# Kernel optimization log

Measured on AMD Instinct MI355X. Metric: run time of the kernel, lower is better.

Reference implementation:

```python
import jax, jax.numpy as jnp
import numpy as np

H = 128             # hidden_channels (heads=1 in PyG HGTConv default)
NT, NC, NM = 150000, 40000, 10000   # transactions, customers, merchants
NE = 150000         # edges per base relation
L = 2               # num HGTConv layers
OUT = 2             # out_channels
# node types: 0=transaction, 1=customer, 2=merchant
EDGE_TYPES = ((1, 0), (2, 0), (0, 1), (0, 2))  # (src_type, dst_type)


def setup_inputs():
    key = jax.random.key(0)
    ks = jax.random.split(key, 20)
    s = 1.0 / np.sqrt(H)
    return {
        'x_tx': jax.random.normal(ks[0], (NT, 16), jnp.float32),
        'x_cust': jax.random.normal(ks[1], (NC, 32), jnp.float32),
        'merch_ids': jnp.arange(NM, dtype=jnp.int32),
        'e_ct_src': jax.random.randint(ks[2], (NE,), 0, NC, dtype=jnp.int32),
        'e_ct_dst': jax.random.randint(ks[3], (NE,), 0, NT, dtype=jnp.int32),
        'e_mt_src': jax.random.randint(ks[4], (NE,), 0, NM, dtype=jnp.int32),
        'e_mt_dst': jax.random.randint(ks[5], (NE,), 0, NT, dtype=jnp.int32),
        'proj_tx_w': jax.random.normal(ks[6], (16, H), jnp.float32) * 0.25,
        'proj_tx_b': jnp.zeros((H,), jnp.float32),
        'proj_cust_w': jax.random.normal(ks[7], (32, H), jnp.float32) * 0.18,
        'proj_cust_b': jnp.zeros((H,), jnp.float32),
        'merch_emb': jax.random.normal(ks[8], (NM, H), jnp.float32),
        'kw': jax.random.normal(ks[9], (L, 3, H, H), jnp.float32) * s,
        'kb': jnp.zeros((L, 3, H), jnp.float32),
        'qw': jax.random.normal(ks[10], (L, 3, H, H), jnp.float32) * s,
        'qb': jnp.zeros((L, 3, H), jnp.float32),
        'vw': jax.random.normal(ks[11], (L, 3, H, H), jnp.float32) * s,
        'vb': jnp.zeros((L, 3, H), jnp.float32),
        'aw': jax.random.normal(ks[12], (L, 3, H, H), jnp.float32) * s,
        'ab': jnp.zeros((L, 3, H), jnp.float32),
        'skip': jnp.ones((L, 3), jnp.float32),
        'a_rel': jax.random.normal(ks[13], (L, 4, H, H), jnp.float32) * s,
        'm_rel': jax.random.normal(ks[14], (L, 4, H, H), jnp.float32) * s,
        'p_rel': jnp.ones((L, 4), jnp.float32),
        'out_w': jax.random.normal(ks[15], (H, OUT), jnp.float32) * s,
        'out_b': jnp.zeros((OUT,), jnp.float32),
    }


def _segment_softmax(alpha, dst, n):
    m = jax.ops.segment_max(alpha, dst, num_segments=n)
    m = jnp.where(jnp.isfinite(m), m, 0.0)
    e = jnp.exp(alpha - m[dst])
    z = jax.ops.segment_sum(e, dst, num_segments=n)
    return e / (z[dst] + 1e-16)


def _hgt_conv(xs, lp, edges, sizes):
    kw, kb, qw, qb, vw, vb, aw, ab, skip, a_rel, m_rel, p_rel = lp
    k = [xs[t] @ kw[t] + kb[t] for t in range(3)]
    q = [xs[t] @ qw[t] + qb[t] for t in range(3)]
    v = [xs[t] @ vw[t] + vb[t] for t in range(3)]
    agg = [jnp.zeros_like(xs[t]) for t in range(3)]
    inv_sqrt_d = 1.0 / jnp.sqrt(jnp.float32(H))
    for r, (st, dt) in enumerate(EDGE_TYPES):
        src, dst = edges[r]
        k_e = (k[st] @ a_rel[r])[src]   # [E,H] relation-transformed keys at edge sources
        v_e = (v[st] @ m_rel[r])[src]   # [E,H]
        a = jnp.sum(q[dt][dst] * k_e, axis=-1) * p_rel[r] * inv_sqrt_d  # [E]
        a = _segment_softmax(a, dst, sizes[dt])
        agg[dt] = agg[dt] + jax.ops.segment_sum(a[:, None] * v_e, dst, num_segments=sizes[dt])
    out = []
    for t in range(3):
        o = jax.nn.gelu(agg[t], approximate=False) @ aw[t] + ab[t]
        beta = jax.nn.sigmoid(skip[t])
        out.append(beta * o + (1.0 - beta) * xs[t])
    return out


def _forward(x_tx, x_cust, proj_tx_w, proj_tx_b, proj_cust_w, proj_cust_b, merch_emb,
             kw, kb, qw, qb, vw, vb, aw, ab, skip, a_rel, m_rel, p_rel, out_w, out_b,
             merch_ids, edges):
    xs = [x_tx @ proj_tx_w + proj_tx_b,
          x_cust @ proj_cust_w + proj_cust_b,
          merch_emb[merch_ids]]
    sizes = (NT, NC, NM)
    for l in range(L):
        lp = (kw[l], kb[l], qw[l], qb[l], vw[l], vb[l], aw[l], ab[l], skip[l],
              a_rel[l], m_rel[l], p_rel[l])
        xs = _hgt_conv(xs, lp, edges, sizes)
        xs = [jax.nn.relu(x) for x in xs]   # dropout is identity in eval mode
    return xs[0] @ out_w + out_b            # logits on 'transaction' nodes


def reference(x_tx, x_cust, merch_ids, e_ct_src, e_ct_dst, e_mt_src, e_mt_dst,
              proj_tx_w, proj_tx_b, proj_cust_w, proj_cust_b, merch_emb,
              kw, kb, qw, qb, vw, vb, aw, ab, skip, a_rel, m_rel, p_rel, out_w, out_b):
    edges = ((e_ct_src, e_ct_dst), (e_mt_src, e_mt_dst),
             (e_ct_dst, e_ct_src), (e_mt_dst, e_mt_src))
    return _forward(x_tx, x_cust, proj_tx_w, proj_tx_b, proj_cust_w, proj_cust_b,
                    merch_emb, kw, kb, qw, qb, vw, vb, aw, ab, skip,
                    a_rel, m_rel, p_rel, out_w, out_b, merch_ids, edges)
```

## Files before the change

kernel.cpp:

```cpp
#include <hip/hip_runtime.h>
#include <math.h>

#define H 128
#define NTX 150000
#define NCU 40000
#define NME 10000
#define NEDGE 150000
#define NLAY 2
#define WC_STRIDE 33280
#define WKC_STRIDE 16640
#define BUF_FLOATS 19200000
#define AGG2_OFF 5120000
#define SCAN_TILE 2048

typedef short s8v __attribute__((ext_vector_type(8)));
typedef float f32x4 __attribute__((ext_vector_type(4)));

__device__ __forceinline__ float gelu_exact(float x) {
    return 0.5f * x * (1.0f + erff(x * 0.70710678118654752f));
}
__device__ __forceinline__ unsigned short f2bf(float x) {
    unsigned u = __float_as_uint(x);
    return (unsigned short)((u + 0x7FFFu + ((u >> 16) & 1u)) >> 16);
}
__device__ __forceinline__ float bf2f(unsigned short b) {
    return __uint_as_float(((unsigned)b) << 16);
}

__global__ __launch_bounds__(256) void fill_val(float* p, int n, float v) {
    int i = blockIdx.x * 256 + threadIdx.x;
    if (i < n) p[i] = v;
}
__global__ __launch_bounds__(256) void zero_int(int* p, int n) {
    int i = blockIdx.x * 256 + threadIdx.x;
    if (i < n) p[i] = 0;
}
__global__ __launch_bounds__(256) void copy_int(int* d, const int* s, int n) {
    int i = blockIdx.x * 256 + threadIdx.x;
    if (i < n) d[i] = s[i];
}

__global__ __launch_bounds__(256) void count_deg(const int* __restrict__ dst,
    int* __restrict__ deg, int E)
{
    int e = blockIdx.x * 256 + threadIdx.x;
    if (e < E) atomicAdd(&deg[dst[e]], 1);
}
__global__ __launch_bounds__(256) void scan1(const int* __restrict__ deg,
    int* __restrict__ out, int* __restrict__ bsum, int n)
{
    __shared__ int ts[256];
    int tid = threadIdx.x;
    int base = blockIdx.x * SCAN_TILE + tid * 8;
    int v[8], pre[8], s = 0;
    #pragma unroll
    for (int j = 0; j < 8; ++j) {
        int idx = base + j;
        v[j] = (idx < n) ? deg[idx] : 0;
        pre[j] = s; s += v[j];
    }
    ts[tid] = s;
    __syncthreads();
    for (int off = 1; off < 256; off <<= 1) {
        int t = (tid >= off) ? ts[tid - off] : 0;
        __syncthreads();
        ts[tid] += t;
        __syncthreads();
    }
    int excl = ts[tid] - s;
    #pragma unroll
    for (int j = 0; j < 8; ++j)
        if (base + j < n) out[base + j] = excl + pre[j];
    if (tid == 255) bsum[blockIdx.x] = ts[255];
}
__global__ __launch_bounds__(64) void scan2(int* __restrict__ bsum, int nb) {
    if (threadIdx.x == 0 && blockIdx.x == 0) {
        int run = 0;
        for (int i = 0; i < nb; ++i) { int t = bsum[i]; bsum[i] = run; run += t; }
    }
}
__global__ __launch_bounds__(256) void scan3(int* __restrict__ out,
    const int* __restrict__ bsum, int n, int total)
{
    int base = blockIdx.x * SCAN_TILE;
    int add = bsum[blockIdx.x];
    for (int j = threadIdx.x; j < SCAN_TILE; j += 256) {
        int k = base + j;
        if (k < n) out[k] += add;
    }
    if (blockIdx.x == 0 && threadIdx.x == 0) out[n] = total;
}
__global__ __launch_bounds__(256) void fill_csr(const int* __restrict__ src,
    const int* __restrict__ dst, int* __restrict__ cursor, int* __restrict__ col, int E)
{
    int e = blockIdx.x * 256 + threadIdx.x;
    if (e >= E) return;
    int pos = atomicAdd(&cursor[dst[e]], 1);
    col[pos] = src[e];
}

template<int K>
__global__ __launch_bounds__(256) void proj_kernel(const float* __restrict__ X,
    const float* __restrict__ W, const float* __restrict__ B,
    float* __restrict__ Y, int N)
{
    __shared__ float Wl[K][128];
    __shared__ float Bl[128];
    int tid = threadIdx.x;
    for (int i = tid; i < K * 128; i += 256) Wl[i >> 7][i & 127] = W[i];
    if (tid < 128) Bl[tid] = B[tid];
    __syncthreads();
    int ng = tid >> 5, lane = tid & 31;
    int n = blockIdx.x * 8 + ng;
    if (n >= N) return;
    const float* xr = X + (size_t)n * K;
    float xa[K];
    #pragma unroll
    for (int k4 = 0; k4 < K / 4; ++k4)
        *(float4*)&xa[k4 * 4] = *(const float4*)(xr + k4 * 4);
    int c0 = lane * 4;
    float4 acc = *(const float4*)&Bl[c0];
    #pragma unroll
    for (int k = 0; k < K; ++k) {
        float4 w = *(const float4*)&Wl[k][c0];
        acc.x += xa[k] * w.x; acc.y += xa[k] * w.y;
        acc.z += xa[k] * w.z; acc.w += xa[k] * w.w;
    }
    *(float4*)(Y + (size_t)n * H + c0) = acc;
}

__global__ __launch_bounds__(256) void gather_rows(const float* __restrict__ src,
    const int* __restrict__ ids, float* __restrict__ dstp, int N)
{
    int t = blockIdx.x * 256 + threadIdx.x;
    if (t >= N * 32) return;
    int n = t >> 5, c4 = t & 31;
    int sid = ids[n];
    ((float4*)dstp)[(size_t)n * 32 + c4] = ((const float4*)src)[(size_t)sid * 32 + c4];
}

__global__ __launch_bounds__(256) void combine1_par(const float* __restrict__ kw,
    const float* __restrict__ kb, const float* __restrict__ vw, const float* __restrict__ vb,
    const float* __restrict__ a_rel, const float* __restrict__ m_rel,
    float* __restrict__ wkc, float* __restrict__ wc)
{
    __shared__ float Rs[64][132];
    int b = blockIdx.x;
    int combo = b >> 3;
    int pass  = (b >> 2) & 1;
    int slice = b & 3;
    int l = combo >> 2, r = combo & 3;
    const int src_t[4] = {1, 2, 0, 0};
    int st = src_t[r];
    const float* Ap = (pass ? vw : kw) + (size_t)(l*3 + st) * H * H;
    const float* Rp = (pass ? m_rel : a_rel) + (size_t)combo * H * H;
    float* Out = pass ? (wc + (size_t)combo * WC_STRIDE + 16384)
                      : (wkc + (size_t)combo * WKC_STRIDE);

    int tid = threadIdx.x;
    int i = slice * 32 + (tid >> 3);
    int jb = tid & 7;
    float acc[16];
    #pragma unroll
    for (int j = 0; j < 16; ++j) acc[j] = 0.f;

    for (int half = 0; half < 2; ++half) {
        __syncthreads();
        for (int idx = tid; idx < 64 * 128; idx += 256)
            Rs[idx >> 7][idx & 127] = Rp[(half * 64 + (idx >> 7)) * H + (idx & 127)];
        __syncthreads();
        for (int k = 0; k < 64; ++k) {
            float a = Ap[i * H + half * 64 + k];
            #pragma unroll
            for (int j = 0; j < 16; ++j) acc[j] += a * Rs[k][jb + j * 8];
        }
    }
    #pragma unroll
    for (int j = 0; j < 16; ++j) Out[i * H + jb + j * 8] = acc[j];

    if (pass == 0 && slice == 0 && tid < 128) {
        const float* Avb = vb + (size_t)(l*3 + st) * H;
        const float* Rv = m_rel + (size_t)combo * H * H;
        float* bvc = wc + (size_t)combo * WC_STRIDE + 32896;
        float s = 0.f;
        for (int k = 0; k < H; ++k) s += Avb[k] * Rv[k * H + tid];
        bvc[tid] = s;
    }
}

__global__ __launch_bounds__(256) void combine2_par(const float* __restrict__ qw,
    const float* __restrict__ qb, const float* __restrict__ wkc, float* __restrict__ wc)
{
    __shared__ float BsT[64][133];
    int b = blockIdx.x;
    int combo = b >> 2;
    int slice = b & 3;
    int l = combo >> 2, r = combo & 3;
    const int dst_t[4] = {0, 0, 1, 2};
    int dt = dst_t[r];
    const float* Q  = qw + (size_t)(l*3 + dt) * H * H;
    const float* Qb = qb + (size_t)(l*3 + dt) * H;
    const float* WKc = wkc + (size_t)combo * WKC_STRIDE;
    float* QWc = wc + (size_t)combo * WC_STRIDE;

    int tid = threadIdx.x;
    int i = slice * 32 + (tid >> 3);
    int jb = tid & 7;
    float acc[16];
    #pragma unroll
    for (int j = 0; j < 16; ++j) acc[j] = 0.f;

    for (int half = 0; half < 2; ++half) {
        __syncthreads();
        for (int idx = tid; idx < 64 * 128; idx += 256) {
            int j = idx >> 6, k = idx & 63;
            BsT[k][j] = WKc[j * H + half * 64 + k];
        }
        __syncthreads();
        for (int k = 0; k < 64; ++k) {
            float a = Q[i * H + half * 64 + k];
            #pragma unroll
            for (int j = 0; j < 16; ++j) acc[j] += a * BsT[k][jb + j * 8];
        }
    }
    #pragma unroll
    for (int j = 0; j < 16; ++j) QWc[i * H + jb + j * 8] = acc[j];

    if (slice == 0 && tid < 128) {
        float* qbc = wc + (size_t)combo * WC_STRIDE + 32768;
        float s = 0.f;
        for (int k = 0; k < H; ++k) s += Qb[k] * WKc[tid * H + k];
        qbc[tid] = s;
    }
}

__global__ __launch_bounds__(256) void wprep(const float* __restrict__ wc,
    const float* __restrict__ aw, unsigned short* __restrict__ wt)
{
    int b = blockIdx.x;
    const float* src = (b < 16)
        ? wc + (size_t)(b >> 1) * WC_STRIDE + ((b & 1) ? 16384 : 0)
        : aw + (size_t)(b - 16) * 16384;
    unsigned short* hi = wt + (size_t)b * 32768;
    unsigned short* lo = hi + 16384;
    for (int idx = threadIdx.x; idx < 16384; idx += 256) {
        int k = idx >> 7, j = idx & 127;
        float w = src[idx];
        unsigned short h = f2bf(w);
        hi[j * 128 + k] = h;
        lo[j * 128 + k] = f2bf(w - bf2f(h));
    }
}

#define STAGE_TILE(SRC, GELU)                                               \
    _Pragma("unroll")                                                       \
    for (int i = 0; i < 8; ++i) {                                           \
        int u = tid + i * 256;                                              \
        int n = u >> 5, c4 = u & 31;                                        \
        int gn = nb + n;                                                    \
        float4 v = make_float4(0.f, 0.f, 0.f, 0.f);                         \
        if (gn < N) v = *(const float4*)((SRC) + (size_t)gn * H + c4 * 4);  \
        if (GELU) {                                                         \
            v.x = gelu_exact(v.x); v.y = gelu_exact(v.y);                   \
            v.z = gelu_exact(v.z); v.w = gelu_exact(v.w);                   \
        }                                                                   \
        ushort4 h, lo;                                                      \
        h.x = f2bf(v.x); lo.x = f2bf(v.x - bf2f(h.x));                      \
        h.y = f2bf(v.y); lo.y = f2bf(v.y - bf2f(h.y));                      \
        h.z = f2bf(v.z); lo.z = f2bf(v.z - bf2f(h.z));                      \
        h.w = f2bf(v.w); lo.w = f2bf(v.w - bf2f(h.w));                      \
        *(ushort4*)&lds[0][n][c4 * 4] = h;                                  \
        *(ushort4*)&lds[1][n][c4 * 4] = lo;                                 \
    }

#define LOAD_BFRAG(WT)                                                      \
    _Pragma("unroll")                                                       \
    for (int n = 0; n < 2; ++n) {                                           \
        int j = col0 + n * 16 + l15;                                        \
        _Pragma("unroll")                                                   \
        for (int kb = 0; kb < 4; ++kb) {                                    \
            bhi[n][kb] = *(const s8v*)((WT) + (size_t)j * 128 + kb * 32 + kg * 8);          \
            blo[n][kb] = *(const s8v*)((WT) + 16384 + (size_t)j * 128 + kb * 32 + kg * 8);  \
        }                                                                   \
    }

#define MFMA_PASS()                                                         \
    _Pragma("unroll")                                                       \
    for (int m = 0; m < 4; ++m) {                                           \
        int row = m * 16 + l15;                                             \
        _Pragma("unroll")                                                   \
        for (int kb = 0; kb < 4; ++kb) {                                    \
            s8v ah = *(const s8v*)&lds[0][row][kb * 32 + kg * 8];           \
            s8v al = *(const s8v*)&lds[1][row][kb * 32 + kg * 8];           \
            _Pragma("unroll")                                               \
            for (int n = 0; n < 2; ++n) {                                   \
                acc[m][n] = __builtin_amdgcn_mfma_f32_16x16x32_bf16(ah, bhi[n][kb], acc[m][n], 0, 0, 0); \
                acc[m][n] = __builtin_amdgcn_mfma_f32_16x16x32_bf16(al, bhi[n][kb], acc[m][n], 0, 0, 0); \
                acc[m][n] = __builtin_amdgcn_mfma_f32_16x16x32_bf16(ah, blo[n][kb], acc[m][n], 0, 0, 0); \
            }                                                               \
        }                                                                   \
    }

template<int MODE>
__global__ __launch_bounds__(256) void mfma_gemm(const float* __restrict__ X,
    const unsigned short* __restrict__ Wt, const float* __restrict__ Bias,
    float* __restrict__ Y, int N, const float* __restrict__ Xold,
    const float* __restrict__ skipP, const float* __restrict__ zb)
{
    __shared__ unsigned short lds[2][64][136];
    int tid = threadIdx.x;
    int nb = blockIdx.x * 64;

    STAGE_TILE(X, MODE == 1)
    __syncthreads();

    int wid = tid >> 6, lane = tid & 63;
    int l15 = lane & 15, kg = lane >> 4;
    int col0 = wid * 32;

    s8v bhi[2][4], blo[2][4];
    LOAD_BFRAG(Wt)

    f32x4 acc[4][2];
    #pragma unroll
    for (int m = 0; m < 4; ++m)
        #pragma unroll
        for (int n = 0; n < 2; ++n)
            acc[m][n] = (f32x4){0.f, 0.f, 0.f, 0.f};

    MFMA_PASS()

    float beta = 0.f, omb = 0.f;
    if (MODE == 1) {
        float s = *skipP;
        beta = 1.f / (1.f + expf(-s));
        omb = 1.f - beta;
    }
    float bias0 = Bias[col0 + l15];
    float bias1 = Bias[col0 + 16 + l15];

    #pragma unroll
    for (int m = 0; m < 4; ++m) {
        #pragma unroll
        for (int r = 0; r < 4; ++r) {
            int grow = nb + m * 16 + kg * 4 + r;
            if (grow < N) {
                float gate = 1.f;
                if (MODE == 3) gate = (zb[grow] > 0.f) ? 1.f : 0.f;
                #pragma unroll
                for (int n = 0; n < 2; ++n) {
                    int col = col0 + n * 16 + l15;
                    float val = acc[m][n][r];
                    float bs = n ? bias1 : bias0;
                    size_t yi = (size_t)grow * H + col;
                    if (MODE == 0) {
                        Y[yi] = val + bs;
                    } else if (MODE == 3) {
                        Y[yi] = val + gate * bs;
                    } else {
                        float o = val + bs;
                        float xo = Xold[yi];
                        Y[yi] = fmaxf(beta * o + omb * xo, 0.f);
                    }
                }
            }
        }
    }
}

__global__ __launch_bounds__(256) void mfma_gemm2q(const float* __restrict__ X,
    const unsigned short* __restrict__ Wt0, const unsigned short* __restrict__ Wt1,
    const float* __restrict__ b0, const float* __restrict__ b1,
    float* __restrict__ Y0, float* __restrict__ Y1, int N)
{
    __shared__ unsigned short lds[2][64][136];
    int tid = threadIdx.x;
    int nb = blockIdx.x * 64;

    STAGE_TILE(X, 0)
    __syncthreads();

    int wid = tid >> 6, lane = tid & 63;
    int l15 = lane & 15, kg = lane >> 4;
    int col0 = wid * 32;

    #pragma unroll
    for (int set = 0; set < 2; ++set) {
        const unsigned short* Wt = set ? Wt1 : Wt0;
        const float* Bias = set ? b1 : b0;
        float* Y = set ? Y1 : Y0;

        s8v bhi[2][4], blo[2][4];
        LOAD_BFRAG(Wt)

        f32x4 acc[4][2];
        #pragma unroll
        for (int m = 0; m < 4; ++m)
            #pragma unroll
            for (int n = 0; n < 2; ++n)
                acc[m][n] = (f32x4){0.f, 0.f, 0.f, 0.f};

        MFMA_PASS()

        float bias0 = Bias[col0 + l15];
        float bias1 = Bias[col0 + 16 + l15];
        #pragma unroll
        for (int m = 0; m < 4; ++m) {
            #pragma unroll
            for (int r = 0; r < 4; ++r) {
                int grow = nb + m * 16 + kg * 4 + r;
                if (grow < N) {
                    #pragma unroll
                    for (int n = 0; n < 2; ++n) {
                        int col = col0 + n * 16 + l15;
                        Y[(size_t)grow * H + col] = acc[m][n][r] + (n ? bias1 : bias0);
                    }
                }
            }
        }
    }
}

__global__ __launch_bounds__(256) void mfma_gemmV2(float* __restrict__ A0,
    const float* __restrict__ A1,
    const unsigned short* __restrict__ Wt0, const unsigned short* __restrict__ Wt1,
    const float* __restrict__ bv0, const float* __restrict__ bv1,
    const float* __restrict__ z0, const float* __restrict__ z1, int N)
{
    __shared__ unsigned short lds[2][64][136];
    int tid = threadIdx.x;
    int nb = blockIdx.x * 64;
    int wid = tid >> 6, lane = tid & 63;
    int l15 = lane & 15, kg = lane >> 4;
    int col0 = wid * 32;

    f32x4 acc[4][2];
    #pragma unroll
    for (int m = 0; m < 4; ++m)
        #pragma unroll
        for (int n = 0; n < 2; ++n)
            acc[m][n] = (f32x4){0.f, 0.f, 0.f, 0.f};

    #pragma unroll
    for (int half = 0; half < 2; ++half) {
        const float* A = half ? A1 : A0;
        const unsigned short* Wt = half ? Wt1 : Wt0;
        if (half) __syncthreads();
        STAGE_TILE(A, 0)
        __syncthreads();
        s8v bhi[2][4], blo[2][4];
        LOAD_BFRAG(Wt)
        MFMA_PASS()
    }

    float b00 = bv0[col0 + l15],  b01 = bv0[col0 + 16 + l15];
    float b10 = bv1[col0 + l15],  b11 = bv1[col0 + 16 + l15];

    #pragma unroll
    for (int m = 0; m < 4; ++m) {
        #pragma unroll
        for (int r = 0; r < 4; ++r) {
            int grow = nb + m * 16 + kg * 4 + r;
            if (grow < N) {
                float g0 = (z0[grow] > 0.f) ? 1.f : 0.f;
                float g1 = (z1[grow] > 0.f) ? 1.f : 0.f;
                #pragma unroll
                for (int n = 0; n < 2; ++n) {
                    int col = col0 + n * 16 + l15;
                    float bs = n ? (g0 * b01 + g1 * b11) : (g0 * b00 + g1 * b10);
                    A0[(size_t)grow * H + col] = acc[m][n][r] + bs;
                }
            }
        }
    }
}

__global__ __launch_bounds__(256) void gather_agg(const int* __restrict__ row_ptr,
    const int* __restrict__ col_idx, float* __restrict__ qtraw,
    const float* __restrict__ xsrc, const float* __restrict__ prel, int ridx,
    float* __restrict__ zout, int ndt)
{
    int g = blockIdx.x * 8 + (threadIdx.x >> 5);
    int lane = threadIdx.x & 31;
    if (g >= ndt) return;
    float4 qv = *(const float4*)(qtraw + (size_t)g * H + lane * 4);
    float scale = prel[ridx] * 0.08838834764831843f;
    int beg = row_ptr[g], end = row_ptr[g + 1];
    float4 acc = make_float4(0.f, 0.f, 0.f, 0.f);
    float z = 0.f;
    for (int i = beg; i < end; ++i) {
        int s = col_idx[i];
        float4 xv = *(const float4*)(xsrc + (size_t)s * H + lane * 4);
        float p = qv.x*xv.x + qv.y*xv.y + qv.z*xv.z + qv.w*xv.w;
        #pragma unroll
        for (int m = 16; m >= 1; m >>= 1) p += __shfl_xor(p, m);
        float ev = expf(p * scale);
        z += ev;
        acc.x += ev * xv.x; acc.y += ev * xv.y;
        acc.z += ev * xv.z; acc.w += ev * xv.w;
    }
    float inv = 1.f / (z + 1e-16f);
    float4 r = make_float4(acc.x * inv, acc.y * inv, acc.z * inv, acc.w * inv);
    *(float4*)(qtraw + (size_t)g * H + lane * 4) = r;
    if (lane == 0) zout[g] = z;
}

__global__ __launch_bounds__(256) void out_kernel(const float* __restrict__ X,
    const float* __restrict__ Wo, const float* __restrict__ bo,
    float* __restrict__ out, int N)
{
    int t = blockIdx.x * 256 + threadIdx.x;
    int n = t >> 5, lane = t & 31;
    if (n >= N) return;
    float4 xv = *(const float4*)(X + (size_t)n * H + lane * 4);
    float xa[4]; *(float4*)xa = xv;
    float p0 = 0.f, p1 = 0.f;
    #pragma unroll
    for (int j = 0; j < 4; ++j) {
        p0 += xa[j] * Wo[(lane*4 + j)*2 + 0];
        p1 += xa[j] * Wo[(lane*4 + j)*2 + 1];
    }
    #pragma unroll
    for (int m = 16; m >= 1; m >>= 1) { p0 += __shfl_xor(p0, m); p1 += __shfl_xor(p1, m); }
    if (lane == 0) {
        out[(size_t)n*2 + 0] = p0 + bo[0];
        out[(size_t)n*2 + 1] = p1 + bo[1];
    }
}

extern "C" void kernel_launch(void* const* d_in, const int* in_sizes, int n_in,
                              void* d_out, int out_size, void* d_ws, size_t ws_size,
                              hipStream_t stream)
{
    const float* x_tx      = (const float*)d_in[0];
    const float* x_cust    = (const float*)d_in[1];
    const int*   merch_ids = (const int*)d_in[2];
    const int*   e_ct_src  = (const int*)d_in[3];
    const int*   e_ct_dst  = (const int*)d_in[4];
    const int*   e_mt_src  = (const int*)d_in[5];
    const int*   e_mt_dst  = (const int*)d_in[6];
    const float* proj_tx_w   = (const float*)d_in[7];
    const float* proj_tx_b   = (const float*)d_in[8];
    const float* proj_cust_w = (const float*)d_in[9];
    const float* proj_cust_b = (const float*)d_in[10];
    const float* merch_emb   = (const float*)d_in[11];
    const float* kw = (const float*)d_in[12];
    const float* kb = (const float*)d_in[13];
    const float* qw = (const float*)d_in[14];
    const float* qb = (const float*)d_in[15];
    const float* vw = (const float*)d_in[16];
    const float* vb = (const float*)d_in[17];
    const float* aw = (const float*)d_in[18];
    const float* ab = (const float*)d_in[19];
    const float* skip  = (const float*)d_in[20];
    const float* a_rel = (const float*)d_in[21];
    const float* m_rel = (const float*)d_in[22];
    const float* p_rel = (const float*)d_in[23];
    const float* out_w = (const float*)d_in[24];
    const float* out_b = (const float*)d_in[25];
    (void)in_sizes; (void)n_in;

    const size_t nsz[3] = {NTX, NCU, NME};

    float* ws = (float*)d_ws;
    size_t off = 0;
    float* xs[3];  for (int t = 0; t < 3; ++t) { xs[t] = ws + off; off += nsz[t]*H; }
    float* bufB    = ws + off; off += BUF_FLOATS;
    float* edgebuf = ws + off; off += BUF_FLOATS;
    float* zbuf0 = ws + off; off += NTX;
    float* zbuf1 = ws + off; off += NTX;
    float* wc   = ws + off; off += 8 * WC_STRIDE;
    float* wkc  = ws + off; off += 8 * WKC_STRIDE;
    int* ibase = (int*)(ws + off);
    const int rp_size[4] = {NTX + 1, NTX + 1, NCU + 1, NME + 1};
    int* rowp[4]; size_t ioff = 0;
    for (int r = 0; r < 4; ++r) { rowp[r] = ibase + ioff; ioff += rp_size[r]; }
    int* colix[4];
    for (int r = 0; r < 4; ++r) { colix[r] = ibase + ioff; ioff += NEDGE; }
    int* cursor = ibase + ioff; ioff += NTX;
    int* bsum   = ibase + ioff; ioff += 256;
    unsigned short* wt = (unsigned short*)(ibase + ioff);
    size_t needed_bytes = off * sizeof(float) + ioff * sizeof(int)
                        + (size_t)22 * 32768 * sizeof(unsigned short);

    if (ws_size < needed_bytes) {
        fill_val<<<(out_size + 255) / 256, 256, 0, stream>>>(
            (float*)d_out, out_size, (float)(ws_size >> 20));
        return;
    }

    const int src_t[4] = {1, 2, 0, 0};
    const int dst_t[4] = {0, 0, 1, 2};
    const int* esrc[4] = {e_ct_src, e_mt_src, e_ct_dst, e_mt_dst};
    const int* edst[4] = {e_ct_dst, e_mt_dst, e_ct_src, e_mt_src};

    const int egrid256 = (NEDGE + 255) / 256;
    for (int r = 0; r < 4; ++r) {
        int ndt = (int)nsz[dst_t[r]];
        int nb = (ndt + SCAN_TILE - 1) / SCAN_TILE;
        zero_int<<<(ndt + 255) / 256, 256, 0, stream>>>(cursor, ndt);
        count_deg<<<egrid256, 256, 0, stream>>>(edst[r], cursor, NEDGE);
        scan1<<<nb, 256, 0, stream>>>(cursor, rowp[r], bsum, ndt);
        scan2<<<1, 64, 0, stream>>>(bsum, nb);
        scan3<<<nb, 256, 0, stream>>>(rowp[r], bsum, ndt, NEDGE);
        copy_int<<<(ndt + 255) / 256, 256, 0, stream>>>(cursor, rowp[r], ndt);
        fill_csr<<<egrid256, 256, 0, stream>>>(esrc[r], edst[r], cursor, colix[r], NEDGE);
    }

    combine1_par<<<64, 256, 0, stream>>>(kw, kb, vw, vb, a_rel, m_rel, wkc, wc);
    combine2_par<<<32, 256, 0, stream>>>(qw, qb, wkc, wc);
    wprep<<<22, 256, 0, stream>>>(wc, aw, wt);

    proj_kernel<16><<<(NTX + 7) / 8, 256, 0, stream>>>(x_tx, proj_tx_w, proj_tx_b, xs[0], NTX);
    proj_kernel<32><<<(NCU + 7) / 8, 256, 0, stream>>>(x_cust, proj_cust_w, proj_cust_b, xs[1], NCU);
    gather_rows<<<(NME * 32 + 255) / 256, 256, 0, stream>>>(merch_emb, merch_ids, xs[2], NME);

    float* aggT[3] = { edgebuf, bufB, bufB + AGG2_OFF };

    for (int l = 0; l < NLAY; ++l) {
        int c0 = l * 4 + 0, c1 = l * 4 + 1;
        const float* W0 = wc + (size_t)c0 * WC_STRIDE;
        const float* W1 = wc + (size_t)c1 * WC_STRIDE;

        mfma_gemm2q<<<(NTX + 63) / 64, 256, 0, stream>>>(
            xs[0], wt + (size_t)(c0*2) * 32768, wt + (size_t)(c1*2) * 32768,
            W0 + 32768, W1 + 32768, edgebuf, bufB, NTX);
        gather_agg<<<(NTX + 7) / 8, 256, 0, stream>>>(
            rowp[0], colix[0], edgebuf, xs[1], p_rel, c0, zbuf0, NTX);
        gather_agg<<<(NTX + 7) / 8, 256, 0, stream>>>(
            rowp[1], colix[1], bufB, xs[2], p_rel, c1, zbuf1, NTX);
        mfma_gemmV2<<<(NTX + 63) / 64, 256, 0, stream>>>(
            edgebuf, bufB, wt + (size_t)(c0*2 + 1) * 32768, wt + (size_t)(c1*2 + 1) * 32768,
            W0 + 32896, W1 + 32896, zbuf0, zbuf1, NTX);

        for (int r = 2; r < 4; ++r) {
            int st = src_t[r], dt = dst_t[r];
            int ndt = (int)nsz[dt];
            int combo = l * 4 + r;
            const float* Wr = wc + (size_t)combo * WC_STRIDE;
            float* buf = aggT[dt];
            int grid = (ndt + 63) / 64;
            mfma_gemm<0><<<grid, 256, 0, stream>>>(
                xs[dt], wt + (size_t)(combo*2) * 32768, Wr + 32768, buf, ndt,
                nullptr, nullptr, nullptr);
            gather_agg<<<(ndt + 7) / 8, 256, 0, stream>>>(
                rowp[r], colix[r], buf, xs[st], p_rel, combo, zbuf0, ndt);
            mfma_gemm<3><<<grid, 256, 0, stream>>>(
                buf, wt + (size_t)(combo*2 + 1) * 32768, Wr + 32896, buf, ndt,
                nullptr, nullptr, zbuf0);
        }

        for (int t = 0; t < 3; ++t)
            mfma_gemm<1><<<(int)((nsz[t] + 63) / 64), 256, 0, stream>>>(
                aggT[t], wt + (size_t)(16 + l*3 + t) * 32768,
                ab + (size_t)(l*3 + t)*H, xs[t], (int)nsz[t],
                xs[t], skip + l*3 + t, nullptr);
    }

    out_kernel<<<(NTX * 32 + 255) / 256, 256, 0, stream>>>(xs[0], out_w, out_b, (float*)d_out, NTX);
}
```

Measured before the change: 1.143 ms.

## Stream weight fragments per k-block, XOR-swizzle LDS, and raise occupancy bound

The MFMA GEMM kernels no longer hold all B fragments in registers up front. Each k-block now loads its B fragments and runs the MFMAs for all four m-tiles, which cuts register pressure. A launch bound of 4 blocks per CU is added to raise occupancy. The LDS tile padding (136 columns) is replaced by an XOR swizzle on the column index (128 columns) to avoid bank conflicts while using less shared memory. The cost is that global weight loads now sit inside the MFMA loop, where they may expose latency.

```diff
diff --git a/kernel.cpp b/kernel.cpp
--- a/kernel.cpp
+++ b/kernel.cpp
@@ -269,45 +269,41 @@
         h.y = f2bf(v.y); lo.y = f2bf(v.y - bf2f(h.y));                      \
         h.z = f2bf(v.z); lo.z = f2bf(v.z - bf2f(h.z));                      \
         h.w = f2bf(v.w); lo.w = f2bf(v.w - bf2f(h.w));                      \
-        *(ushort4*)&lds[0][n][c4 * 4] = h;                                  \
-        *(ushort4*)&lds[1][n][c4 * 4] = lo;                                 \
-    }
-
-#define LOAD_BFRAG(WT)                                                      \
+        int sc = (c4 * 4) ^ ((n & 7) << 3);                                 \
+        *(ushort4*)&lds[0][n][sc] = h;                                      \
+        *(ushort4*)&lds[1][n][sc] = lo;                                     \
+    }
+
+#define MFMA_TILE64(WT)                                                     \
     _Pragma("unroll")                                                       \
-    for (int n = 0; n < 2; ++n) {                                           \
-        int j = col0 + n * 16 + l15;                                        \
+    for (int kb = 0; kb < 4; ++kb) {                                        \
+        const unsigned short* wp = (WT) + kb * 32 + kg * 8;                 \
+        s8v bh0 = *(const s8v*)(wp + (size_t)(col0 + l15) * 128);           \
+        s8v bh1 = *(const s8v*)(wp + (size_t)(col0 + 16 + l15) * 128);      \
+        s8v bl0 = *(const s8v*)(wp + 16384 + (size_t)(col0 + l15) * 128);   \
+        s8v bl1 = *(const s8v*)(wp + 16384 + (size_t)(col0 + 16 + l15) * 128); \
         _Pragma("unroll")                                                   \
-        for (int kb = 0; kb < 4; ++kb) {                                    \
-            bhi[n][kb] = *(const s8v*)((WT) + (size_t)j * 128 + kb * 32 + kg * 8);          \
-            blo[n][kb] = *(const s8v*)((WT) + 16384 + (size_t)j * 128 + kb * 32 + kg * 8);  \
+        for (int m = 0; m < 4; ++m) {                                       \
+            int row = m * 16 + l15;                                         \
+            int offx = (kb * 32 + kg * 8) ^ ((row & 7) << 3);               \
+            s8v ah = *(const s8v*)&lds[0][row][offx];                       \
+            s8v al = *(const s8v*)&lds[1][row][offx];                       \
+            acc[m][0] = __builtin_amdgcn_mfma_f32_16x16x32_bf16(ah, bh0, acc[m][0], 0, 0, 0); \
+            acc[m][0] = __builtin_amdgcn_mfma_f32_16x16x32_bf16(al, bh0, acc[m][0], 0, 0, 0); \
+            acc[m][0] = __builtin_amdgcn_mfma_f32_16x16x32_bf16(ah, bl0, acc[m][0], 0, 0, 0); \
+            acc[m][1] = __builtin_amdgcn_mfma_f32_16x16x32_bf16(ah, bh1, acc[m][1], 0, 0, 0); \
+            acc[m][1] = __builtin_amdgcn_mfma_f32_16x16x32_bf16(al, bh1, acc[m][1], 0, 0, 0); \
+            acc[m][1] = __builtin_amdgcn_mfma_f32_16x16x32_bf16(ah, bl1, acc[m][1], 0, 0, 0); \
         }                                                                   \
     }
 
-#define MFMA_PASS()                                                         \
-    _Pragma("unroll")                                                       \
-    for (int m = 0; m < 4; ++m) {                                           \
-        int row = m * 16 + l15;                                             \
-        _Pragma("unroll")                                                   \
-        for (int kb = 0; kb < 4; ++kb) {                                    \
-            s8v ah = *(const s8v*)&lds[0][row][kb * 32 + kg * 8];           \
-            s8v al = *(const s8v*)&lds[1][row][kb * 32 + kg * 8];           \
-            _Pragma("unroll")                                               \
-            for (int n = 0; n < 2; ++n) {                                   \
-                acc[m][n] = __builtin_amdgcn_mfma_f32_16x16x32_bf16(ah, bhi[n][kb], acc[m][n], 0, 0, 0); \
-                acc[m][n] = __builtin_amdgcn_mfma_f32_16x16x32_bf16(al, bhi[n][kb], acc[m][n], 0, 0, 0); \
-                acc[m][n] = __builtin_amdgcn_mfma_f32_16x16x32_bf16(ah, blo[n][kb], acc[m][n], 0, 0, 0); \
-            }                                                               \
-        }                                                                   \
-    }
-
 template<int MODE>
-__global__ __launch_bounds__(256) void mfma_gemm(const float* __restrict__ X,
+__global__ __launch_bounds__(256, 4) void mfma_gemm(const float* __restrict__ X,
     const unsigned short* __restrict__ Wt, const float* __restrict__ Bias,
     float* __restrict__ Y, int N, const float* __restrict__ Xold,
     const float* __restrict__ skipP, const float* __restrict__ zb)
 {
-    __shared__ unsigned short lds[2][64][136];
+    __shared__ unsigned short lds[2][64][128];
     int tid = threadIdx.x;
     int nb = blockIdx.x * 64;
 
@@ -317,9 +313,6 @@
     int wid = tid >> 6, lane = tid & 63;
     int l15 = lane & 15, kg = lane >> 4;
     int col0 = wid * 32;
-
-    s8v bhi[2][4], blo[2][4];
-    LOAD_BFRAG(Wt)
 
     f32x4 acc[4][2];
     #pragma unroll
@@ -328,7 +321,7 @@
         for (int n = 0; n < 2; ++n)
             acc[m][n] = (f32x4){0.f, 0.f, 0.f, 0.f};
 
-    MFMA_PASS()
+    MFMA_TILE64(Wt)
 
     float beta = 0.f, omb = 0.f;
     if (MODE == 1) {
@@ -368,12 +361,12 @@
     }
 }
 
-__global__ __launch_bounds__(256) void mfma_gemm2q(const float* __restrict__ X,
+__global__ __launch_bounds__(256, 4) void mfma_gemm2q(const float* __restrict__ X,
     const unsigned short* __restrict__ Wt0, const unsigned short* __restrict__ Wt1,
     const float* __restrict__ b0, const float* __restrict__ b1,
     float* __restrict__ Y0, float* __restrict__ Y1, int N)
 {
-    __shared__ unsigned short lds[2][64][136];
+    __shared__ unsigned short lds[2][64][128];
     int tid = threadIdx.x;
     int nb = blockIdx.x * 64;
 
@@ -389,9 +382,6 @@
         const unsigned short* Wt = set ? Wt1 : Wt0;
         const float* Bias = set ? b1 : b0;
         float* Y = set ? Y1 : Y0;
-
-        s8v bhi[2][4], blo[2][4];
-        LOAD_BFRAG(Wt)
 
         f32x4 acc[4][2];
         #pragma unroll
@@ -400,7 +390,7 @@
             for (int n = 0; n < 2; ++n)
                 acc[m][n] = (f32x4){0.f, 0.f, 0.f, 0.f};
 
-        MFMA_PASS()
+        MFMA_TILE64(Wt)
 
         float bias0 = Bias[col0 + l15];
         float bias1 = Bias[col0 + 16 + l15];
@@ -421,13 +411,13 @@
     }
 }
 
-__global__ __launch_bounds__(256) void mfma_gemmV2(float* __restrict__ A0,
+__global__ __launch_bounds__(256, 4) void mfma_gemmV2(float* __restrict__ A0,
     const float* __restrict__ A1,
     const unsigned short* __restrict__ Wt0, const unsigned short* __restrict__ Wt1,
     const float* __restrict__ bv0, const float* __restrict__ bv1,
     const float* __restrict__ z0, const float* __restrict__ z1, int N)
 {
-    __shared__ unsigned short lds[2][64][136];
+    __shared__ unsigned short lds[2][64][128];
     int tid = threadIdx.x;
     int nb = blockIdx.x * 64;
     int wid = tid >> 6, lane = tid & 63;
@@ -441,16 +431,17 @@
         for (int n = 0; n < 2; ++n)
             acc[m][n] = (f32x4){0.f, 0.f, 0.f, 0.f};
 
-    #pragma unroll
-    for (int half = 0; half < 2; ++half) {
-        const float* A = half ? A1 : A0;
-        const unsigned short* Wt = half ? Wt1 : Wt0;
-        if (half) __syncthreads();
+    {
+        STAGE_TILE(A0, 0)
+        __syncthreads();
+        MFMA_TILE64(Wt0)
+    }
+    __syncthreads();
+    {
+        const float* A = A1;
         STAGE_TILE(A, 0)
         __syncthreads();
-        s8v bhi[2][4], blo[2][4];
-        LOAD_BFRAG(Wt)
-        MFMA_PASS()
+        MFMA_TILE64(Wt1)
     }
 
     float b00 = bv0[col0 + l15],  b01 = bv0[col0 + 16 + l15];
```

Measured after the change: 1.111 ms (median of 2 runs). 1.03x faster.
